# Kernel optimization log

Measured on AMD Instinct MI355X. Metric: run time of the kernel, lower is better.

The kernel has to match this reference:

```python
import jax, jax.numpy as jnp
import numpy as np

DIM = 768
HEADS = 12
TOPK = 32


def setup_inputs() -> dict:
    key = jax.random.key(0)
    k1, k2, k3 = jax.random.split(key, 3)
    B, hw, T = 8, 576, 4
    N = hw + T * hw
    x = jax.random.normal(k1, (B, N, DIM), dtype=jnp.float32)
    qkv_w = jax.random.normal(k2, (3 * DIM, DIM), dtype=jnp.float32) * 0.02
    proj_w = jax.random.normal(k3, (DIM, DIM), dtype=jnp.float32) * 0.02
    proj_b = jnp.zeros((DIM,), dtype=jnp.float32)
    return {"x": x, "qkv_w": qkv_w, "proj_w": proj_w, "proj_b": proj_b, "T": T, "hw": hw}


def _query_topk_every_frame(attn, hw, T):
    # attn: [B, H, hw, hw + T*hw]
    B, H, n1, _ = attn.shape
    qa = attn[..., :hw]                       # [B,H,hw,hw] query self part
    ma = attn[..., hw:].reshape(B, H, n1, T, hw)  # per-frame memory scores
    vals, idx = jax.lax.top_k(ma, TOPK)       # [B,H,hw,T,K]
    cat = jnp.concatenate([qa, vals.reshape(B, H, n1, T * TOPK)], axis=-1)
    sm = jax.nn.softmax(cat, axis=-1)         # softmax over hw + T*K survivors
    qa2 = sm[..., :hw]
    tv = sm[..., hw:].reshape(B, H, n1, T, TOPK)
    # scatter normalized top-k values back into dense per-frame affinity
    bi = jnp.arange(B)[:, None, None, None, None]
    hi = jnp.arange(H)[None, :, None, None, None]
    ni = jnp.arange(n1)[None, None, :, None, None]
    ti = jnp.arange(T)[None, None, None, :, None]
    aff = jnp.zeros_like(ma).at[bi, hi, ni, ti, idx].set(tv)
    return jnp.concatenate([qa2, aff.reshape(B, H, n1, T * hw)], axis=-1)


def reference(x, qkv_w, proj_w, proj_b, T, hw):
    B, N, C = x.shape
    assert N == hw + T * hw
    hd = C // HEADS
    scale = hd ** -0.5
    qkv = (x @ qkv_w.T).reshape(B, N, 3, HEADS, hd).transpose(2, 0, 3, 1, 4)
    q, k, v = qkv[0], qkv[1], qkv[2]          # each [B,H,N,hd]
    query_q = q[:, :, :hw]                    # [B,H,hw,hd]
    attn = jnp.einsum('bhqd,bhkd->bhqk', query_q, k) * scale  # [B,H,hw,N]
    attn = _query_topk_every_frame(attn, hw, T)
    out = jnp.einsum('bhqk,bhkd->bhqd', attn, v)  # [B,H,hw,hd]
    query = out.transpose(0, 2, 1, 3).reshape(B, hw, C)
    query = query @ proj_w.T + proj_b
    # memory tokens pass through unchanged
    return jnp.concatenate([query, x[:, hw:]], axis=1)
```

## Files before the change

kernel.cpp:

```cpp
#include <hip/hip_runtime.h>
#include <hip/hip_bf16.h>


using s16x8 = __attribute__((ext_vector_type(8))) short;
using f32x4 = __attribute__((ext_vector_type(4))) float;
typedef unsigned short u16;
typedef unsigned int u32;

#define MFMA_B16(A,B,C) __builtin_amdgcn_mfma_f32_16x16x32_bf16(A,B,C,0,0,0)

__device__ __forceinline__ u16 f2bf(float f) {
  unsigned u = __float_as_uint(f);
  u += 0x7FFFu + ((u >> 16) & 1u);
  return (u16)(u >> 16);
}
__device__ __forceinline__ float bf2f(u16 h) {
  return __uint_as_float(((unsigned)h) << 16);
}
__device__ __forceinline__ int lanes_below(unsigned long long m) {
  return __builtin_amdgcn_mbcnt_hi((unsigned)(m >> 32),
         __builtin_amdgcn_mbcnt_lo((unsigned)m, 0));
}
__device__ __forceinline__ void stage16(const u16* __restrict__ g, u16* l) {
  __builtin_amdgcn_global_load_lds(
      (const __attribute__((address_space(1))) unsigned int*)g,
      (__attribute__((address_space(3))) unsigned int*)l, 16, 0, 0);
}
__device__ __forceinline__ float sumpair(u32 d) {
  return __uint_as_float(d << 16) + __uint_as_float(d & 0xFFFF0000u);
}

__global__ __launch_bounds__(256) void cvt_kernel(const float* __restrict__ src,
                                                  u16* __restrict__ dst, int n4) {
  int i = blockIdx.x * blockDim.x + threadIdx.x;
  if (i >= n4) return;
  float4 v = ((const float4*)src)[i];
  unsigned lo = (unsigned)f2bf(v.x) | ((unsigned)f2bf(v.y) << 16);
  unsigned hi = (unsigned)f2bf(v.z) | ((unsigned)f2bf(v.w) << 16);
  uint2 o; o.x = lo; o.y = hi;
  ((uint2*)dst)[i] = o;
}

__global__ __launch_bounds__(256) void copy_tail_kernel(const float* __restrict__ x,
                                                        float* __restrict__ out) {
  int i = blockIdx.x * blockDim.x + threadIdx.x;
  int b = i / 442368;
  int off = i - b * 442368;
  size_t e = (size_t)b * 552960 + 110592 + off;
  ((float4*)out)[e] = ((const float4*)x)[e];
}

template<int MODE>
__global__ __launch_bounds__(256) void gemm_nt(
    const u16* __restrict__ A, const u16* __restrict__ Bw,
    const float* __restrict__ bias,
    u16* __restrict__ qbuf, u16* __restrict__ kbuf,
    u16* __restrict__ vtb, float* __restrict__ fout)
{
  __shared__ __align__(16) u16 smem[128 * 128];
  u16* sA = smem;
  u16* sB = smem + 128 * 64;
  const int n0 = blockIdx.x * 128;
  const int m0 = blockIdx.y * 128;
  if (MODE == 0 && n0 < 768) {
    const int s = m0 % 2880;
    if (s >= 576 && s + 128 <= 2880) return;
  }
  const int tid = threadIdx.x;
  const int w = tid >> 6, lane = tid & 63;
  const int l15 = lane & 15, rg = lane >> 4;
  const int ko = rg * 8;
  const int mq = (w >> 1) * 64, nq = (w & 1) * 64;
  const int trow = tid >> 3, tcol = (tid & 7) * 8;

  f32x4 z = {0.f, 0.f, 0.f, 0.f};
  f32x4 acc[4][4];
  #pragma unroll
  for (int i = 0; i < 4; ++i)
    #pragma unroll
    for (int j = 0; j < 4; ++j) acc[i][j] = z;

  for (int k0 = 0; k0 < 768; k0 += 64) {
    __syncthreads();
    #pragma unroll
    for (int i = 0; i < 4; ++i) {
      stage16(&A[(size_t)(m0 + trow + i * 32) * 768 + k0 + tcol],
              &sA[(trow + i * 32) * 64 + tcol]);
      stage16(&Bw[(size_t)(n0 + trow + i * 32) * 768 + k0 + tcol],
              &sB[(trow + i * 32) * 64 + tcol]);
    }
    __syncthreads();
    #pragma unroll
    for (int kk = 0; kk < 2; ++kk) {
      const int ko2 = kk * 32 + ko;
      s16x8 af[4], bf[4];
      #pragma unroll
      for (int i = 0; i < 4; ++i) {
        af[i] = *(const s16x8*)&sA[(mq + i * 16 + l15) * 64 + ko2];
        bf[i] = *(const s16x8*)&sB[(nq + i * 16 + l15) * 64 + ko2];
      }
      #pragma unroll
      for (int mi = 0; mi < 4; ++mi)
        #pragma unroll
        for (int ni = 0; ni < 4; ++ni)
          acc[mi][ni] = MFMA_B16(af[mi], bf[ni], acc[mi][ni]);
    }
  }

  if (MODE == 0) {
    const int which = n0 / 768;
    const int nb = n0 % 768;
    if (which == 2) {
      __syncthreads();
      #pragma unroll
      for (int mi = 0; mi < 4; ++mi)
        #pragma unroll
        for (int ni = 0; ni < 4; ++ni)
          #pragma unroll
          for (int r = 0; r < 4; ++r)
            smem[(mq + mi * 16 + rg * 4 + r) * 128 + nq + ni * 16 + l15] =
                f2bf(acc[mi][ni][r]);
      __syncthreads();
      const int c = tid & 127, kh = tid >> 7;
      const int gm0 = m0 + kh * 64;
      const int bb = gm0 / 2880, rr0 = gm0 - bb * 2880;
      const int ng = nb + c;
      const int hh = ng >> 6, dd = ng & 63;
      u16* dst = vtb + ((size_t)((bb * 12 + hh) * 64 + dd)) * 2880 + rr0;
      #pragma unroll
      for (int seg = 0; seg < 4; ++seg) {
        u16 tmp[16];
        #pragma unroll
        for (int i = 0; i < 16; ++i)
          tmp[i] = smem[(kh * 64 + seg * 16 + i) * 128 + c];
        *(int4*)&dst[seg * 16]     = *(const int4*)&tmp[0];
        *(int4*)&dst[seg * 16 + 8] = *(const int4*)&tmp[8];
      }
    } else {
      #pragma unroll
      for (int mi = 0; mi < 4; ++mi)
        #pragma unroll
        for (int ni = 0; ni < 4; ++ni)
          #pragma unroll
          for (int r = 0; r < 4; ++r) {
            const int gm = m0 + mq + mi * 16 + rg * 4 + r;
            const int b  = gm / 2880;
            const int rr = gm - b * 2880;
            const int ng = nb + nq + ni * 16 + l15;
            const int h  = ng >> 6, d = ng & 63;
            const float cc = acc[mi][ni][r];
            if (which == 0) {
              if (rr < 576)
                qbuf[((size_t)(b * 12 + h) * 576 + rr) * 64 + d] = f2bf(cc * 0.125f);
            } else {
              kbuf[((size_t)(b * 12 + h) * 2880 + rr) * 64 + d] = f2bf(cc);
            }
          }
    }
  } else {
    #pragma unroll
    for (int mi = 0; mi < 4; ++mi)
      #pragma unroll
      for (int ni = 0; ni < 4; ++ni)
        #pragma unroll
        for (int r = 0; r < 4; ++r) {
          const int gm = m0 + mq + mi * 16 + rg * 4 + r;
          const int gn = n0 + nq + ni * 16 + l15;
          const int b = gm / 576;
          const int q = gm - b * 576;
          fout[((size_t)b * 2880 + q) * 768 + gn] = acc[mi][ni][r] + bias[gn];
        }
  }
}

__global__ __launch_bounds__(256, 7) void attn_kernel(
    const u16* __restrict__ qbuf, const u16* __restrict__ kbuf,
    const u16* __restrict__ vtb,
    float* __restrict__ opart, float* __restrict__ dpart)
{
  constexpr int PST = 648;
  constexpr int BIAS = 0x3E80;
  __shared__ __align__(16) u16 s_p[16 * PST];

  const int bid = blockIdx.x;
  const int L = (bid & 7) * 2160 + (bid >> 3);
  const int b   = L / 2160;
  const int rm  = L % 2160;
  const int c   = rm / 432;
  const int h   = (rm / 36) % 12;
  const int qt  = rm % 36;
  const int bh = b * 12 + h;
  const int q0 = qt * 16;
  const int bq = bh * 36 + qt;
  const int tid = threadIdx.x, w = tid >> 6, lane = tid & 63;
  const int l15 = lane & 15, rg = lane >> 4;
  const int ko = rg * 8;

  #pragma unroll
  for (int i = 0; i < 2; ++i) {
    const int idx = tid + 256 * i;
    const int row = idx >> 5, dw = idx & 31;
    *(u32*)&s_p[row * PST + 576 + dw * 2] = 0u;
  }

  const u16* qp = qbuf + ((size_t)bh * 576 + q0) * 64;
  s16x8 aQ[2];
  aQ[0] = *(const s16x8*)&qp[l15 * 64 + ko];
  aQ[1] = *(const s16x8*)&qp[l15 * 64 + 32 + ko];

  const u16* kp = kbuf + (size_t)bh * 2880 * 64;
  const u16* vt = vtb + ((size_t)bh * 64 + w * 16 + l15) * 2880;
  f32x4 zz = {0.f, 0.f, 0.f, 0.f};
  f32x4 accO = zz;

  #pragma unroll 3
  for (int t = 0; t < 9; ++t) {
    const int wk = w * 144 + t * 16;
    const u16* kr = kp + (size_t)(c * 576 + wk + l15) * 64 + ko;
    s16x8 kf0 = *(const s16x8*)&kr[0];
    s16x8 kf1 = *(const s16x8*)&kr[32];
    f32x4 a0 = zz;
    a0 = MFMA_B16(aQ[0], kf0, a0);
    a0 = MFMA_B16(aQ[1], kf1, a0);
    #pragma unroll
    for (int r = 0; r < 4; ++r)
      s_p[(rg * 4 + r) * PST + wk + l15] =
          (u16)(__float_as_uint(__expf(a0[r])) >> 16);
  }
  __syncthreads();

  if (c == 0) {
    #pragma unroll
    for (int ri = 0; ri < 4; ++ri) {
      const int q = w * 4 + ri;
      const u32* rp = (const u32*)&s_p[q * PST];
      uint4 dv = *(const uint4*)&rp[lane * 4];
      u32 tl = rp[256 + lane];
      float s = sumpair(dv.x) + sumpair(dv.y) + sumpair(dv.z) + sumpair(dv.w)
              + sumpair(tl);
      #pragma unroll
      for (int off = 1; off < 64; off <<= 1) s += __shfl_xor(s, off);
      if (lane == 0) dpart[(size_t)(bq * 5 + c) * 16 + q] = s;
    }
  } else {
    #pragma unroll
    for (int rp2 = 0; rp2 < 2; ++rp2) {
      const int qA = w * 4 + rp2 * 2, qB = qA + 1;
      u32* rpA = (u32*)&s_p[qA * PST];
      u32* rpB = (u32*)&s_p[qB * PST];
      unsigned kA[10], kB[10];
      {
        uint4 dA = *(const uint4*)&rpA[lane * 4];
        uint4 dB = *(const uint4*)&rpB[lane * 4];
        u32 tA = rpA[256 + lane], tB = rpB[256 + lane];
        kA[0]=dA.x&0xFFFF; kA[1]=dA.x>>16; kA[2]=dA.y&0xFFFF; kA[3]=dA.y>>16;
        kA[4]=dA.z&0xFFFF; kA[5]=dA.z>>16; kA[6]=dA.w&0xFFFF; kA[7]=dA.w>>16;
        kA[8]=tA&0xFFFF;   kA[9]=tA>>16;
        kB[0]=dB.x&0xFFFF; kB[1]=dB.x>>16; kB[2]=dB.y&0xFFFF; kB[3]=dB.y>>16;
        kB[4]=dB.z&0xFFFF; kB[5]=dB.z>>16; kB[6]=dB.w&0xFFFF; kB[7]=dB.w>>16;
        kB[8]=tB&0xFFFF;   kB[9]=tB>>16;
      }
      #pragma unroll
      for (int j = 0; j < 10; ++j) {
        int tA2 = (int)kA[j] - BIAS;
        int tB2 = (int)kB[j] - BIAS;
        kA[j] = (unsigned)(tA2 < 0 ? 0 : (tA2 > 1023 ? 1023 : tA2));
        kB[j] = (unsigned)(tB2 < 0 ? 0 : (tB2 > 1023 ? 1023 : tB2));
      }
      unsigned pfA = 0, pfB = 0;
      #pragma unroll
      for (int bit = 9; bit >= 0; --bit) {
        const unsigned cA = pfA | (1u << bit), cB = pfB | (1u << bit);
        u32 cnt = 0;
        #pragma unroll
        for (int j = 0; j < 10; ++j) {
          cnt += (kA[j] >= cA) ? 1u : 0u;
          cnt += (kB[j] >= cB) ? 0x10000u : 0u;
        }
        #pragma unroll
        for (int off = 1; off < 64; off <<= 1)
          cnt += __shfl_xor(cnt, off);
        pfA = ((cnt & 0xFFFFu) >= 32u) ? cA : pfA;
        pfB = ((cnt >> 16)    >= 32u) ? cB : pfB;
      }
      #pragma unroll
      for (int rr = 0; rr < 2; ++rr) {
        const unsigned* k = rr ? kB : kA;
        const unsigned pf = rr ? pfB : pfA;
        u32* rp = rr ? rpB : rpA;
        const int q = rr ? qB : qA;
        int cnt_gt = 0;
        #pragma unroll
        for (int j = 0; j < 10; ++j)
          cnt_gt += __popcll(__ballot(k[j] > pf));
        const int rem = 32 - cnt_gt;
        int run_eq = 0;
        u32 wd[5];
        float dsum = 0.f;
        #pragma unroll
        for (int j2 = 0; j2 < 5; ++j2) {
          u32 packed = 0;
          #pragma unroll
          for (int h2 = 0; h2 < 2; ++h2) {
            const int j = j2 * 2 + h2;
            const unsigned kj = k[j];
            unsigned long long eq = __ballot(kj == pf);
            const bool sel = (kj > pf) ||
                (kj == pf && run_eq + lanes_below(eq) < rem);
            run_eq += __popcll(eq);
            const u32 w16 = sel ? (kj + (u32)BIAS) : 0u;
            packed |= w16 << (16 * h2);
          }
          wd[j2] = packed;
          dsum += sumpair(packed);
        }
        *(uint4*)&rp[lane * 4] = *(const uint4*)&wd[0];
        rp[256 + lane] = wd[4];
        #pragma unroll
        for (int off = 1; off < 64; off <<= 1) dsum += __shfl_xor(dsum, off);
        if (lane == 0) dpart[(size_t)(bq * 5 + c) * 16 + q] = dsum;
      }
    }
    __syncthreads();
  }

  #pragma unroll 3
  for (int k0 = 0; k0 < 576; k0 += 32) {
    s16x8 vf = *(const s16x8*)&vt[(size_t)c * 576 + k0 + ko];
    s16x8 pa = *(const s16x8*)&s_p[l15 * PST + k0 + ko];
    accO = MFMA_B16(pa, vf, accO);
  }

  float* op = opart + (size_t)(bq * 5 + c) * 1024;
  const int d = w * 16 + l15;
  #pragma unroll
  for (int r = 0; r < 4; ++r) {
    const int row = rg * 4 + r;
    op[row * 64 + d] = accO[r];
  }
}

__global__ __launch_bounds__(256) void attn_reduce(
    const float* __restrict__ opart, const float* __restrict__ dpart,
    u16* __restrict__ aout)
{
  const int bq = blockIdx.x;
  const int t = threadIdx.x;
  const int b = bq / 432;
  const int h = (bq / 36) % 12;
  const int qt = bq % 36;
  const float* ob = opart + (size_t)bq * 5 * 1024;
  const float* db = dpart + (size_t)bq * 5 * 16;
  #pragma unroll
  for (int k2 = 0; k2 < 4; ++k2) {
    const int e = t + k2 * 256;
    const int row = e >> 6, d = e & 63;
    float o = 0.f, dn = 0.f;
    #pragma unroll
    for (int c = 0; c < 5; ++c) {
      o  += ob[c * 1024 + e];
      dn += db[c * 16 + row];
    }
    aout[((size_t)(b * 576 + qt * 16 + row)) * 768 + h * 64 + d] = f2bf(o / dn);
  }
}

extern "C" void kernel_launch(void* const* d_in, const int* in_sizes, int n_in,
                              void* d_out, int out_size, void* d_ws, size_t ws_size,
                              hipStream_t stream)
{
  const float* x      = (const float*)d_in[0];
  const float* qkv_w  = (const float*)d_in[1];
  const float* proj_w = (const float*)d_in[2];
  const float* proj_b = (const float*)d_in[3];
  float* out = (float*)d_out;

  char* ws = (char*)d_ws;
  size_t off = 0;
  auto alloc = [&](size_t bytes) -> void* {
    void* p = ws + off;
    off += (bytes + 255) & ~(size_t)255;
    return p;
  };
  u16* xb    = (u16*)alloc((size_t)23040 * 768 * 2);
  u16* wqb   = (u16*)alloc((size_t)2304 * 768 * 2);
  u16* wpb   = (u16*)alloc((size_t)768 * 768 * 2);
  u16* qbuf  = (u16*)alloc((size_t)96 * 576 * 64 * 2);
  u16* vtb   = (u16*)alloc((size_t)96 * 64 * 2880 * 2);
  u16* aout  = (u16*)alloc((size_t)4608 * 768 * 2);
  float* opart = (float*)alloc((size_t)17280 * 1024 * 4);
  float* dpart = (float*)alloc((size_t)17280 * 16 * 4);
  u16* kbuf = (u16*)d_out;

  cvt_kernel<<<17280, 256, 0, stream>>>(x, xb, 17694720 / 4);
  cvt_kernel<<<1728, 256, 0, stream>>>(qkv_w, wqb, 1769472 / 4);
  cvt_kernel<<<576, 256, 0, stream>>>(proj_w, wpb, 589824 / 4);
  gemm_nt<0><<<dim3(18, 180), 256, 0, stream>>>(xb, wqb, nullptr,
                                                qbuf, kbuf, vtb, nullptr);
  attn_kernel<<<17280, 256, 0, stream>>>(qbuf, kbuf, vtb, opart, dpart);
  attn_reduce<<<3456, 256, 0, stream>>>(opart, dpart, aout);
  gemm_nt<1><<<dim3(6, 36), 256, 0, stream>>>(aout, wpb, proj_b,
                                              nullptr, nullptr, nullptr, out);
  copy_tail_kernel<<<13824, 256, 0, stream>>>(x, out);
}
```

Before: 486.4 us.

## Store attention partials in bf16 and batch top-k radix select over four rows

Attention partial outputs are now written as bf16 instead of fp32, which halves the opart write and read traffic between attn_kernel and attn_reduce. The reduce kernel is vectorized so each thread handles four contiguous elements and multiplies by a reciprocal instead of dividing. The top-k radix select now processes all four rows of a wave together, using ballot/popcount counts in place of the packed shuffle reductions, and batches the final denominator shuffles. The cost is extra rounding of the partial sums before the final normalization, plus higher register pressure from holding 40 keys per lane.

Result: slower. 527.6 us (+8.5%).

```diff
diff --git a/kernel.cpp b/kernel.cpp
--- a/kernel.cpp
+++ b/kernel.cpp
@@ -176,7 +176,7 @@
 __global__ __launch_bounds__(256, 7) void attn_kernel(
     const u16* __restrict__ qbuf, const u16* __restrict__ kbuf,
     const u16* __restrict__ vtb,
-    float* __restrict__ opart, float* __restrict__ dpart)
+    u16* __restrict__ opart, float* __restrict__ dpart)
 {
   constexpr int PST = 648;
   constexpr int BIAS = 0x3E80;
@@ -243,83 +243,86 @@
       if (lane == 0) dpart[(size_t)(bq * 5 + c) * 16 + q] = s;
     }
   } else {
-    #pragma unroll
-    for (int rp2 = 0; rp2 < 2; ++rp2) {
-      const int qA = w * 4 + rp2 * 2, qB = qA + 1;
-      u32* rpA = (u32*)&s_p[qA * PST];
-      u32* rpB = (u32*)&s_p[qB * PST];
-      unsigned kA[10], kB[10];
-      {
-        uint4 dA = *(const uint4*)&rpA[lane * 4];
-        uint4 dB = *(const uint4*)&rpB[lane * 4];
-        u32 tA = rpA[256 + lane], tB = rpB[256 + lane];
-        kA[0]=dA.x&0xFFFF; kA[1]=dA.x>>16; kA[2]=dA.y&0xFFFF; kA[3]=dA.y>>16;
-        kA[4]=dA.z&0xFFFF; kA[5]=dA.z>>16; kA[6]=dA.w&0xFFFF; kA[7]=dA.w>>16;
-        kA[8]=tA&0xFFFF;   kA[9]=tA>>16;
-        kB[0]=dB.x&0xFFFF; kB[1]=dB.x>>16; kB[2]=dB.y&0xFFFF; kB[3]=dB.y>>16;
-        kB[4]=dB.z&0xFFFF; kB[5]=dB.z>>16; kB[6]=dB.w&0xFFFF; kB[7]=dB.w>>16;
-        kB[8]=tB&0xFFFF;   kB[9]=tB>>16;
+    u32 key[4][10];
+    #pragma unroll
+    for (int ri = 0; ri < 4; ++ri) {
+      const u32* rp = (const u32*)&s_p[(w * 4 + ri) * PST];
+      uint4 dv = *(const uint4*)&rp[lane * 4];
+      u32 tl = rp[256 + lane];
+      key[ri][0]=dv.x&0xFFFF; key[ri][1]=dv.x>>16;
+      key[ri][2]=dv.y&0xFFFF; key[ri][3]=dv.y>>16;
+      key[ri][4]=dv.z&0xFFFF; key[ri][5]=dv.z>>16;
+      key[ri][6]=dv.w&0xFFFF; key[ri][7]=dv.w>>16;
+      key[ri][8]=tl&0xFFFF;   key[ri][9]=tl>>16;
+    }
+    #pragma unroll
+    for (int ri = 0; ri < 4; ++ri)
+      #pragma unroll
+      for (int j = 0; j < 10; ++j) {
+        const int t2 = (int)key[ri][j] - BIAS;
+        key[ri][j] = (u32)(t2 < 0 ? 0 : (t2 > 1023 ? 1023 : t2));
       }
-      #pragma unroll
-      for (int j = 0; j < 10; ++j) {
-        int tA2 = (int)kA[j] - BIAS;
-        int tB2 = (int)kB[j] - BIAS;
-        kA[j] = (unsigned)(tA2 < 0 ? 0 : (tA2 > 1023 ? 1023 : tA2));
-        kB[j] = (unsigned)(tB2 < 0 ? 0 : (tB2 > 1023 ? 1023 : tB2));
+    u32 pf[4] = {0u, 0u, 0u, 0u};
+    #pragma unroll
+    for (int bit = 9; bit >= 0; --bit) {
+      int cnt[4];
+      #pragma unroll
+      for (int ri = 0; ri < 4; ++ri) {
+        const u32 cand = pf[ri] | (1u << bit);
+        int cn = 0;
+        #pragma unroll
+        for (int j = 0; j < 10; ++j)
+          cn += __popcll(__ballot(key[ri][j] >= cand));
+        cnt[ri] = cn;
       }
-      unsigned pfA = 0, pfB = 0;
-      #pragma unroll
-      for (int bit = 9; bit >= 0; --bit) {
-        const unsigned cA = pfA | (1u << bit), cB = pfB | (1u << bit);
-        u32 cnt = 0;
-        #pragma unroll
-        for (int j = 0; j < 10; ++j) {
-          cnt += (kA[j] >= cA) ? 1u : 0u;
-          cnt += (kB[j] >= cB) ? 0x10000u : 0u;
+      #pragma unroll
+      for (int ri = 0; ri < 4; ++ri)
+        if (cnt[ri] >= 32) pf[ri] |= (1u << bit);
+    }
+    float ds4[4];
+    #pragma unroll
+    for (int ri = 0; ri < 4; ++ri) {
+      const u32 pfx = pf[ri];
+      int cnt_gt = 0;
+      #pragma unroll
+      for (int j = 0; j < 10; ++j)
+        cnt_gt += __popcll(__ballot(key[ri][j] > pfx));
+      const int rem = 32 - cnt_gt;
+      int run_eq = 0;
+      u32 wd[5];
+      float dsum = 0.f;
+      #pragma unroll
+      for (int j2 = 0; j2 < 5; ++j2) {
+        u32 packed = 0;
+        #pragma unroll
+        for (int h2 = 0; h2 < 2; ++h2) {
+          const int j = j2 * 2 + h2;
+          const u32 kj = key[ri][j];
+          unsigned long long eq = __ballot(kj == pfx);
+          const bool sel = (kj > pfx) ||
+              (kj == pfx && run_eq + lanes_below(eq) < rem);
+          run_eq += __popcll(eq);
+          const u32 w16 = sel ? (kj + (u32)BIAS) : 0u;
+          packed |= w16 << (16 * h2);
         }
-        #pragma unroll
-        for (int off = 1; off < 64; off <<= 1)
-          cnt += __shfl_xor(cnt, off);
-        pfA = ((cnt & 0xFFFFu) >= 32u) ? cA : pfA;
-        pfB = ((cnt >> 16)    >= 32u) ? cB : pfB;
+        wd[j2] = packed;
+        dsum += sumpair(packed);
       }
-      #pragma unroll
-      for (int rr = 0; rr < 2; ++rr) {
-        const unsigned* k = rr ? kB : kA;
-        const unsigned pf = rr ? pfB : pfA;
-        u32* rp = rr ? rpB : rpA;
-        const int q = rr ? qB : qA;
-        int cnt_gt = 0;
-        #pragma unroll
-        for (int j = 0; j < 10; ++j)
-          cnt_gt += __popcll(__ballot(k[j] > pf));
-        const int rem = 32 - cnt_gt;
-        int run_eq = 0;
-        u32 wd[5];
-        float dsum = 0.f;
-        #pragma unroll
-        for (int j2 = 0; j2 < 5; ++j2) {
-          u32 packed = 0;
-          #pragma unroll
-          for (int h2 = 0; h2 < 2; ++h2) {
-            const int j = j2 * 2 + h2;
-            const unsigned kj = k[j];
-            unsigned long long eq = __ballot(kj == pf);
-            const bool sel = (kj > pf) ||
-                (kj == pf && run_eq + lanes_below(eq) < rem);
-            run_eq += __popcll(eq);
-            const u32 w16 = sel ? (kj + (u32)BIAS) : 0u;
-            packed |= w16 << (16 * h2);
-          }
-          wd[j2] = packed;
-          dsum += sumpair(packed);
-        }
-        *(uint4*)&rp[lane * 4] = *(const uint4*)&wd[0];
-        rp[256 + lane] = wd[4];
-        #pragma unroll
-        for (int off = 1; off < 64; off <<= 1) dsum += __shfl_xor(dsum, off);
-        if (lane == 0) dpart[(size_t)(bq * 5 + c) * 16 + q] = dsum;
-      }
+      u32* rp = (u32*)&s_p[(w * 4 + ri) * PST];
+      *(uint4*)&rp[lane * 4] = *(const uint4*)&wd[0];
+      rp[256 + lane] = wd[4];
+      ds4[ri] = dsum;
+    }
+    #pragma unroll
+    for (int off = 1; off < 64; off <<= 1) {
+      #pragma unroll
+      for (int ri = 0; ri < 4; ++ri)
+        ds4[ri] += __shfl_xor(ds4[ri], off);
+    }
+    if (lane == 0) {
+      #pragma unroll
+      for (int ri = 0; ri < 4; ++ri)
+        dpart[(size_t)(bq * 5 + c) * 16 + w * 4 + ri] = ds4[ri];
     }
     __syncthreads();
   }
@@ -331,17 +334,17 @@
     accO = MFMA_B16(pa, vf, accO);
   }
 
-  float* op = opart + (size_t)(bq * 5 + c) * 1024;
+  u16* op = opart + (size_t)(bq * 5 + c) * 1024;
   const int d = w * 16 + l15;
   #pragma unroll
   for (int r = 0; r < 4; ++r) {
     const int row = rg * 4 + r;
-    op[row * 64 + d] = accO[r];
+    op[row * 64 + d] = f2bf(accO[r]);
   }
 }
 
 __global__ __launch_bounds__(256) void attn_reduce(
-    const float* __restrict__ opart, const float* __restrict__ dpart,
+    const u16* __restrict__ opart, const float* __restrict__ dpart,
     u16* __restrict__ aout)
 {
   const int bq = blockIdx.x;
@@ -349,20 +352,25 @@
   const int b = bq / 432;
   const int h = (bq / 36) % 12;
   const int qt = bq % 36;
-  const float* ob = opart + (size_t)bq * 5 * 1024;
+  const u16* ob = opart + (size_t)bq * 5 * 1024;
   const float* db = dpart + (size_t)bq * 5 * 16;
+  const int e = t * 4;
+  const int row = e >> 6, d0 = e & 63;
+  float dn = 0.f;
   #pragma unroll
-  for (int k2 = 0; k2 < 4; ++k2) {
-    const int e = t + k2 * 256;
-    const int row = e >> 6, d = e & 63;
-    float o = 0.f, dn = 0.f;
-    #pragma unroll
-    for (int c = 0; c < 5; ++c) {
-      o  += ob[c * 1024 + e];
-      dn += db[c * 16 + row];
-    }
-    aout[((size_t)(b * 576 + qt * 16 + row)) * 768 + h * 64 + d] = f2bf(o / dn);
-  }
+  for (int c = 0; c < 5; ++c) dn += db[c * 16 + row];
+  float o0 = 0.f, o1 = 0.f, o2 = 0.f, o3 = 0.f;
+  #pragma unroll
+  for (int c = 0; c < 5; ++c) {
+    uint2 v = *(const uint2*)&ob[c * 1024 + e];
+    o0 += bf2f((u16)(v.x & 0xFFFF)); o1 += bf2f((u16)(v.x >> 16));
+    o2 += bf2f((u16)(v.y & 0xFFFF)); o3 += bf2f((u16)(v.y >> 16));
+  }
+  const float inv = 1.f / dn;
+  uint2 ov;
+  ov.x = (u32)f2bf(o0 * inv) | ((u32)f2bf(o1 * inv) << 16);
+  ov.y = (u32)f2bf(o2 * inv) | ((u32)f2bf(o3 * inv) << 16);
+  *(uint2*)&aout[((size_t)(b * 576 + qt * 16 + row)) * 768 + h * 64 + d0] = ov;
 }
 
 extern "C" void kernel_launch(void* const* d_in, const int* in_sizes, int n_in,
@@ -388,7 +396,7 @@
   u16* qbuf  = (u16*)alloc((size_t)96 * 576 * 64 * 2);
   u16* vtb   = (u16*)alloc((size_t)96 * 64 * 2880 * 2);
   u16* aout  = (u16*)alloc((size_t)4608 * 768 * 2);
-  float* opart = (float*)alloc((size_t)17280 * 1024 * 4);
+  u16* opart = (u16*)alloc((size_t)17280 * 1024 * 2);
   float* dpart = (float*)alloc((size_t)17280 * 16 * 4);
   u16* kbuf = (u16*)d_out;
 
```
